# Performance work log

Hardware: AMD Instinct MI355X
Metric: run time of the kernel (lower is better)

The kernel has to match this reference:

```python
import jax, jax.numpy as jnp
import numpy as np
import math

HEAD_NUM = 16


def setup_inputs() -> dict:
    key = jax.random.key(0)
    ks = jax.random.split(key, 6)
    B, S, E = 2, 2048, 1024
    sc = 1.0 / math.sqrt(E)
    return {
        "x": jax.random.normal(ks[0], (B, S, E), dtype=jnp.float32),
        "mask": jnp.ones((B, S), dtype=jnp.int32),
        "Wq": jax.random.normal(ks[1], (E, E), dtype=jnp.float32) * sc,
        "bq": jnp.zeros((E,), dtype=jnp.float32),
        "Wk": jax.random.normal(ks[2], (E, E), dtype=jnp.float32) * sc,
        "bk": jnp.zeros((E,), dtype=jnp.float32),
        "Wv": jax.random.normal(ks[3], (E, E), dtype=jnp.float32) * sc,
        "bv": jnp.zeros((E,), dtype=jnp.float32),
        "Wo": jax.random.normal(ks[4], (E, E), dtype=jnp.float32) * sc,
        "bo": jnp.zeros((E,), dtype=jnp.float32),
    }


def reference(x, mask, Wq, bq, Wk, bk, Wv, bv, Wo, bo):
    B, S, E = x.shape
    H = HEAD_NUM
    D = E // H
    # Projections (nn.Linear: x @ W^T + b; W here stored so that x @ W is equivalent)
    q = (x @ Wq + bq).reshape(B, S, H, D).transpose(0, 2, 1, 3)  # [B,H,S,D]
    k = (x @ Wk + bk).reshape(B, S, H, D).transpose(0, 2, 1, 3)
    v = (x @ Wv + bv).reshape(B, S, H, D).transpose(0, 2, 1, 3)
    score = jnp.einsum("bhqd,bhkd->bhqk", q, k) / jnp.sqrt(jnp.asarray(D, x.dtype))
    # Faithful to source: masked positions (mask==0) are filled with +inf
    m = mask[:, None, None, :]  # [B,1,1,S]
    score = jnp.where(m == 0, jnp.inf, score)
    attn = jax.nn.softmax(score, axis=-1)
    # dropout is identity in eval mode
    out = jnp.einsum("bhqk,bhkd->bhqd", attn, v)
    out = out.transpose(0, 2, 1, 3).reshape(B, S, E)
    return out @ Wo + bo
```

## Files before the change

### kernel.cpp

```cpp
#include <hip/hip_runtime.h>
#include <hip/hip_bf16.h>
#include <math.h>


#define S_LEN 2048
#define EMB   1024
#define HN    16
#define HD    64
#define BATCH 2
#define MROWS (BATCH * S_LEN)
#define NEL   ((size_t)MROWS * EMB)

typedef _Float16 f16x8 __attribute__((ext_vector_type(8)));
typedef _Float16 f16x4 __attribute__((ext_vector_type(4)));
typedef _Float16 f16x2 __attribute__((ext_vector_type(2)));
typedef float    f32x4  __attribute__((ext_vector_type(4)));
typedef float    f32x16 __attribute__((ext_vector_type(16)));
typedef unsigned u32x4  __attribute__((ext_vector_type(4)));

#define GLOAD_LDS16(g, l) \
  __builtin_amdgcn_global_load_lds((const __attribute__((address_space(1))) void*)(g), \
                                   (__attribute__((address_space(3))) void*)(l), 16, 0, 0)

__device__ __forceinline__ float exp2fast(float x) {
#if __has_builtin(__builtin_amdgcn_exp2f)
  return __builtin_amdgcn_exp2f(x);
#else
  return __expf(x * 0.69314718056f);
#endif
}

__device__ __forceinline__ unsigned pk_f16(float a, float b) {
#if __has_builtin(__builtin_amdgcn_cvt_pkrtz)
  auto h = __builtin_amdgcn_cvt_pkrtz(a, b);
  return __builtin_bit_cast(unsigned, h);
#else
  unsigned lo = (unsigned)__builtin_bit_cast(unsigned short, (_Float16)a);
  unsigned hi = (unsigned)__builtin_bit_cast(unsigned short, (_Float16)b);
  return lo | (hi << 16);
#endif
}

__device__ __forceinline__ float dot2acc(unsigned p, float acc) {
#if __has_builtin(__builtin_amdgcn_fdot2)
  f16x2 ones = {(_Float16)1.0f, (_Float16)1.0f};
  return __builtin_amdgcn_fdot2(__builtin_bit_cast(f16x2, p), ones, acc, false);
#else
  f16x2 v = __builtin_bit_cast(f16x2, p);
  return acc + (float)v[0] + (float)v[1];
#endif
}

__device__ __forceinline__ f32x16 mfma32(f16x8 a, f16x8 b, f32x16 c) {
  return __builtin_amdgcn_mfma_f32_32x32x16_f16(a, b, c, 0, 0, 0);
}

__global__ __launch_bounds__(256)
void prep_f16(const float* __restrict__ x,
              const float* __restrict__ Wq, const float* __restrict__ Wk,
              const float* __restrict__ Wv, const float* __restrict__ Wo,
              _Float16* __restrict__ xf, _Float16* __restrict__ Wt,
              _Float16* __restrict__ Wot) {
  __shared__ float tile[64][65];
  const int bid = blockIdx.x;
  const int tt  = threadIdx.x;
  if (bid < 2048) {
    const int i = bid * 256 + tt;
    const float4* s = (const float4*)x + (size_t)i * 2;
    float4 a = s[0], b = s[1];
    f16x8 o = {(_Float16)a.x, (_Float16)a.y, (_Float16)a.z, (_Float16)a.w,
               (_Float16)b.x, (_Float16)b.y, (_Float16)b.z, (_Float16)b.w};
    *((f16x8*)xf + i) = o;
    return;
  }
  const int j   = bid - 2048;
  const int job = j >> 8;
  const int tl  = j & 255;
  const int bn  = (tl & 15) * 64, bk = (tl >> 4) * 64;
  const float* W = (job == 0) ? Wq : (job == 1) ? Wk : (job == 2) ? Wv : Wo;
  _Float16* dst = (job == 3) ? Wot : Wt + (size_t)job * EMB * EMB;
  const int c = tt & 63, r4 = tt >> 6;
#pragma unroll
  for (int jj = 0; jj < 16; ++jj) {
    int r = r4 * 16 + jj;
    tile[r][c] = W[(size_t)(bk + r) * EMB + bn + c];
  }
  __syncthreads();
#pragma unroll
  for (int jj = 0; jj < 16; ++jj) {
    int rr = r4 * 16 + jj;
    dst[(size_t)(bn + rr) * EMB + bk + c] = (_Float16)tile[c][rr];
  }
}

template<bool SW>
__device__ __forceinline__ void gemm_kloop(
    const _Float16* __restrict__ gA, const _Float16* __restrict__ gB,
    _Float16* As, _Float16* Bs, int tid, int wr, int wc, int ql, int hi,
    f32x16 (&acc)[2][2]) {
#define GSTAGE(buf, k0) do { \
    _Pragma("unroll") \
    for (int j = 0; j < 2; ++j) { \
      const int c = tid + j * 256; \
      const int row = c >> 2; \
      const int sl = ((c & 3) ^ (row & 3) ^ ((row >> 2) & 3)) * 8; \
      GLOAD_LDS16(gA + (size_t)row * EMB + (k0) + sl, As + (buf) * 4096 + c * 8); \
      GLOAD_LDS16(gB + (size_t)row * EMB + (k0) + sl, Bs + (buf) * 4096 + c * 8); \
    } \
  } while (0)
#define GCOMP(bufc) do { \
    const _Float16* Ab = As + (bufc) * 4096; \
    const _Float16* Bb = Bs + (bufc) * 4096; \
    _Pragma("unroll") \
    for (int ks = 0; ks < 2; ++ks) { \
      const int sl = ((((ks << 1) | hi) ^ (ql & 3) ^ ((ql >> 2) & 3)) << 3); \
      f16x8 a0 = *(const f16x8*)&Ab[(wr * 64 + ql) * 32 + sl]; \
      f16x8 a1 = *(const f16x8*)&Ab[(wr * 64 + 32 + ql) * 32 + sl]; \
      f16x8 b0 = *(const f16x8*)&Bb[(wc * 64 + ql) * 32 + sl]; \
      f16x8 b1 = *(const f16x8*)&Bb[(wc * 64 + 32 + ql) * 32 + sl]; \
      if (SW) { \
        acc[0][0] = mfma32(b0, a0, acc[0][0]); \
        acc[0][1] = mfma32(b1, a0, acc[0][1]); \
        acc[1][0] = mfma32(b0, a1, acc[1][0]); \
        acc[1][1] = mfma32(b1, a1, acc[1][1]); \
      } else { \
        acc[0][0] = mfma32(a0, b0, acc[0][0]); \
        acc[0][1] = mfma32(a0, b1, acc[0][1]); \
        acc[1][0] = mfma32(a1, b0, acc[1][0]); \
        acc[1][1] = mfma32(a1, b1, acc[1][1]); \
      } \
    } \
  } while (0)

  GSTAGE(0, 0);
  GSTAGE(1, 32);
  int cur = 0, stg = 2;
#pragma unroll 1
  for (int t = 0; t < 31; ++t) {
    asm volatile("s_waitcnt vmcnt(4) lgkmcnt(0)" ::: "memory");
    __builtin_amdgcn_sched_barrier(0);
    __builtin_amdgcn_s_barrier();
    __builtin_amdgcn_sched_barrier(0);
    if (t < 30) GSTAGE(stg, (t + 2) * 32);
    GCOMP(cur);
    cur = (cur == 2) ? 0 : cur + 1;
    stg = (stg == 2) ? 0 : stg + 1;
  }
  asm volatile("s_waitcnt vmcnt(0) lgkmcnt(0)" ::: "memory");
  __builtin_amdgcn_sched_barrier(0);
  __builtin_amdgcn_s_barrier();
  __builtin_amdgcn_sched_barrier(0);
  GCOMP(cur);
#undef GCOMP
#undef GSTAGE
}

template<int MODE>
__global__ __launch_bounds__(256, 3)
void gemm_f16(const _Float16* __restrict__ A, const _Float16* __restrict__ Bt,
              int Ncols,
              _Float16* __restrict__ qf, _Float16* __restrict__ kf,
              _Float16* __restrict__ vf, float* __restrict__ outF,
              const float* __restrict__ b0, const float* __restrict__ b1,
              const float* __restrict__ b2) {
  __shared__ _Float16 As[3 * 128 * 32];
  __shared__ _Float16 Bs[3 * 128 * 32];
  const int tid  = threadIdx.x;
  const int lane = tid & 63, w = tid >> 6;
  const int ql = lane & 31, hi = lane >> 5;
  const int wr = w >> 1, wc = w & 1;

  const int nbx  = Ncols >> 7;
  const int ncpx = nbx >> 3;
  const int xcd  = blockIdx.x & 7;
  const int idx  = blockIdx.x >> 3;
  const int col0 = (xcd * ncpx + idx % ncpx) << 7;
  const int row0 = (idx / ncpx) << 7;

  f32x16 acc[2][2];
#pragma unroll
  for (int mi = 0; mi < 2; ++mi)
#pragma unroll
    for (int ni = 0; ni < 2; ++ni) acc[mi][ni] = (f32x16){};

  const _Float16* gA = A  + (size_t)row0 * EMB;
  const _Float16* gB = Bt + (size_t)col0 * EMB;

  const bool is_v = (MODE == 0) && (col0 >= 2048);
  if (is_v) gemm_kloop<true >(gA, gB, As, Bs, tid, wr, wc, ql, hi, acc);
  else      gemm_kloop<false>(gA, gB, As, Bs, tid, wr, wc, ql, hi, acc);

  if (MODE == 1) {
#pragma unroll
    for (int mi = 0; mi < 2; ++mi)
#pragma unroll
      for (int ni = 0; ni < 2; ++ni) {
        const int n = col0 + wc * 64 + ni * 32 + ql;
        const float bias = b0[n];
#pragma unroll
        for (int r = 0; r < 16; ++r) {
          const int m = row0 + wr * 64 + mi * 32 + (r & 3) + 8 * (r >> 2) + 4 * hi;
          outF[(size_t)m * EMB + n] = acc[mi][ni][r] + bias;
        }
      }
  } else if (!is_v) {
#pragma unroll
    for (int mi = 0; mi < 2; ++mi)
#pragma unroll
      for (int ni = 0; ni < 2; ++ni) {
        const int n = col0 + wc * 64 + ni * 32 + ql;
        const int mat = n >> 10, e = n & 1023;
        const float bias = (mat == 0 ? b0 : b1)[e];
        const int h = e >> 6, d = e & 63;
#pragma unroll
        for (int r = 0; r < 16; ++r) {
          const int m = row0 + wr * 64 + mi * 32 + (r & 3) + 8 * (r >> 2) + 4 * hi;
          const int bb = m >> 11, ss = m & 2047;
          const int bh = bb * HN + h;
          float val = acc[mi][ni][r] + bias;
          if (mat == 0) {
            qf[((size_t)bh * S_LEN + ss) * HD + d] = (_Float16)(val * 0.18033688f);
          } else {
            kf[((size_t)bh * S_LEN + ss) * HD + d] = (_Float16)val;
          }
        }
      }
  } else {
#pragma unroll
    for (int mi = 0; mi < 2; ++mi) {
      const int m = row0 + wr * 64 + mi * 32 + ql;
      const int bb = m >> 11, ss = m & 2047;
      const int ssp = (ss & ~12) | ((ss & 4) << 1) | ((ss & 8) >> 1);
#pragma unroll
      for (int ni = 0; ni < 2; ++ni) {
#pragma unroll
        for (int r = 0; r < 16; ++r) {
          const int n = col0 + wc * 64 + ni * 32 + (r & 3) + 8 * (r >> 2) + 4 * hi;
          const int e = n - 2048;
          const int h = e >> 6, d = e & 63;
          const int bh = bb * HN + h;
          float val = acc[mi][ni][r] + b2[e];
          vf[((size_t)bh * HD + d) * S_LEN + ssp] = (_Float16)val;
        }
      }
    }
  }
}

__global__ __launch_bounds__(512)
void attn_f16v5(const _Float16* __restrict__ Qf, const _Float16* __restrict__ Kf,
                const _Float16* __restrict__ VfT, _Float16* __restrict__ Of) {
  __shared__ _Float16 SH[2][4][4096];

  const int tid  = threadIdx.x;
  const int lane = tid & 63, w = tid >> 6;
  const int ws4  = w & 3, ks = w >> 2;
  const int ql = lane & 31;
  const int hi = lane >> 5;

  const int logical = ((blockIdx.x & 7) << 6) | (blockIdx.x >> 3);
  const int bh = logical >> 4;
  const int qc = logical & 15;
  const int q0w = (qc << 7) + (ws4 << 5);
  const int kbase = ks << 10;

  const size_t qbase = ((size_t)bh * S_LEN + q0w + ql) * HD + hi * 8;
  f16x8 qa[4];
#pragma unroll
  for (int ds = 0; ds < 4; ++ds) qa[ds] = *(const f16x8*)&Qf[qbase + ds * 16];

  f32x16 o0 = {}, o1 = {};
  float lsum = 0.f;

  const int cA = (ws4 << 6) + lane, cB = cA + 256;
  const int rA = cA >> 3, sA = ((cA & 7) ^ (rA & 7)) * 8;
  const int rB = cB >> 3, sB = ((cB & 7) ^ (rB & 7)) * 8;
  const _Float16* KB = Kf  + (size_t)bh * S_LEN * HD;
  const _Float16* VB = VfT + (size_t)bh * HD * S_LEN;

#pragma unroll 1
  for (int t = 0; t < 8; ++t) {
    const int k0 = kbase + t * 128;
    __syncthreads();
    GLOAD_LDS16(KB + (size_t)(k0 + rA) * HD + sA,       &SH[ks][0][cA * 8]);
    GLOAD_LDS16(KB + (size_t)(k0 + rB) * HD + sB,       &SH[ks][0][cB * 8]);
    GLOAD_LDS16(KB + (size_t)(k0 + 64 + rA) * HD + sA,  &SH[ks][1][cA * 8]);
    GLOAD_LDS16(KB + (size_t)(k0 + 64 + rB) * HD + sB,  &SH[ks][1][cB * 8]);
    GLOAD_LDS16(VB + (size_t)rA * S_LEN + k0 + sA,      &SH[ks][2][cA * 8]);
    GLOAD_LDS16(VB + (size_t)rB * S_LEN + k0 + sB,      &SH[ks][2][cB * 8]);
    GLOAD_LDS16(VB + (size_t)rA * S_LEN + k0 + 64 + sA, &SH[ks][3][cA * 8]);
    GLOAD_LDS16(VB + (size_t)rB * S_LEN + k0 + 64 + sB, &SH[ks][3][cB * 8]);
    __syncthreads();

#pragma unroll
    for (int kh = 0; kh < 2; ++kh) {
      const _Float16* Kt = &SH[ks][kh][0];
      const _Float16* Vt = &SH[ks][2 + kh][0];
      f32x16 sf0 = {}, sf1 = {};
#pragma unroll
      for (int ds = 0; ds < 4; ++ds) {
        const int sl = ((ds * 2 + hi) ^ (ql & 7)) * 8;
        f16x8 ka0 = *(const f16x8*)&Kt[ql * 64 + sl];
        f16x8 ka1 = *(const f16x8*)&Kt[(32 + ql) * 64 + sl];
        sf0 = mfma32(ka0, qa[ds], sf0);
        sf1 = mfma32(ka1, qa[ds], sf1);
      }

      unsigned wv[16];
#pragma unroll
      for (int i = 0; i < 8; ++i) {
        float p0 = exp2fast(sf0[2 * i]), p1 = exp2fast(sf0[2 * i + 1]);
        float p2 = exp2fast(sf1[2 * i]), p3 = exp2fast(sf1[2 * i + 1]);
        wv[i]     = pk_f16(p0, p1);
        wv[8 + i] = pk_f16(p2, p3);
        lsum = dot2acc(wv[i], lsum);
        lsum = dot2acc(wv[8 + i], lsum);
      }

#pragma unroll
      for (int kq = 0; kq < 4; ++kq) {
        u32x4 pw = {wv[4 * kq], wv[4 * kq + 1], wv[4 * kq + 2], wv[4 * kq + 3]};
        f16x8 pb = __builtin_bit_cast(f16x8, pw);
        const int sl = ((kq * 2 + hi) ^ (ql & 7)) * 8;
        f16x8 va0 = *(const f16x8*)&Vt[ql * 64 + sl];
        f16x8 va1 = *(const f16x8*)&Vt[(32 + ql) * 64 + sl];
        o0 = mfma32(va0, pb, o0);
        o1 = mfma32(va1, pb, o1);
      }
    }
  }

  __syncthreads();
  float* CMB = reinterpret_cast<float*>(&SH[0][0][0]);
  float* slot = CMB + ((size_t)((ws4 << 6) + lane)) * 36;
  if (ks == 1) {
#pragma unroll
    for (int t = 0; t < 4; ++t) {
      *(f32x4*)&slot[4 * t] =
          (f32x4){o0[4 * t], o0[4 * t + 1], o0[4 * t + 2], o0[4 * t + 3]};
      *(f32x4*)&slot[16 + 4 * t] =
          (f32x4){o1[4 * t], o1[4 * t + 1], o1[4 * t + 2], o1[4 * t + 3]};
    }
    slot[32] = lsum;
  }
  __syncthreads();
  if (ks == 0) {
#pragma unroll
    for (int t = 0; t < 4; ++t) {
      f32x4 a0 = *(const f32x4*)&slot[4 * t];
      f32x4 a1 = *(const f32x4*)&slot[16 + 4 * t];
#pragma unroll
      for (int j = 0; j < 4; ++j) { o0[4 * t + j] += a0[j]; o1[4 * t + j] += a1[j]; }
    }
    lsum += slot[32];
    float lt  = lsum + __shfl_xor(lsum, 32);
    float inv = 1.0f / lt;
    const int b = bh >> 4, h = bh & 15;
    _Float16* ob = Of + ((size_t)(b * S_LEN + q0w + ql)) * EMB + (h << 6);
#pragma unroll
    for (int t = 0; t < 4; ++t) {
      f16x4 v0, v1;
#pragma unroll
      for (int j = 0; j < 4; ++j) {
        v0[j] = (_Float16)(o0[4 * t + j] * inv);
        v1[j] = (_Float16)(o1[4 * t + j] * inv);
      }
      *(f16x4*)&ob[8 * t + 4 * hi]      = v0;
      *(f16x4*)&ob[32 + 8 * t + 4 * hi] = v1;
    }
  }
}


extern "C" void kernel_launch(void* const* d_in, const int* in_sizes, int n_in,
                              void* d_out, int out_size, void* d_ws, size_t ws_size,
                              hipStream_t stream) {
  const float* x  = (const float*)d_in[0];
  const float* Wq = (const float*)d_in[2];
  const float* bq = (const float*)d_in[3];
  const float* Wk = (const float*)d_in[4];
  const float* bk = (const float*)d_in[5];
  const float* Wv = (const float*)d_in[6];
  const float* bv = (const float*)d_in[7];
  const float* Wo = (const float*)d_in[8];
  const float* bo = (const float*)d_in[9];
  float* out = (float*)d_out;

  _Float16* Qf  = (_Float16*)d_ws;
  _Float16* Kf  = Qf + NEL;
  _Float16* VfT = Kf + NEL;
  _Float16* xf  = VfT + NEL;
  _Float16* Of  = xf;
  _Float16* Wt  = xf + NEL;
  _Float16* Wot = Wt + 3 * (size_t)EMB * EMB;

  prep_f16<<<dim3(3072), 256, 0, stream>>>(x, Wq, Wk, Wv, Wo, xf, Wt, Wot);

  gemm_f16<0><<<dim3((MROWS / 128) * (3072 / 128)), 256, 0, stream>>>(
      xf, Wt, 3072, Qf, Kf, VfT, nullptr, bq, bk, bv);

  attn_f16v5<<<dim3(BATCH * HN * (S_LEN / 128)), 512, 0, stream>>>(
      Qf, Kf, VfT, Of);

  gemm_f16<1><<<dim3((MROWS / 128) * (EMB / 128)), 256, 0, stream>>>(
      Of, Wot, 1024, nullptr, nullptr, nullptr, out, bo, nullptr, nullptr);
}
```

Before: 115.3 us.

## Load K tiles directly into registers instead of staging through LDS

The attention kernel now reads K fragments straight from global memory into registers, and prefetches the second half-tile of K during the first half's compute. Only V is staged through shared memory, which halves LDS usage and the number of async LDS loads per iteration. The softmax row-sum is also split into two independent accumulators to shorten the dependency chain. In exchange, every wave reads K from global/L2 separately with no cross-wave reuse, and register pressure rises.

```diff
diff --git a/kernel.cpp b/kernel.cpp
--- a/kernel.cpp
+++ b/kernel.cpp
@@ -248,9 +248,9 @@
 }
 
 __global__ __launch_bounds__(512)
-void attn_f16v5(const _Float16* __restrict__ Qf, const _Float16* __restrict__ Kf,
+void attn_f16v8(const _Float16* __restrict__ Qf, const _Float16* __restrict__ Kf,
                 const _Float16* __restrict__ VfT, _Float16* __restrict__ Of) {
-  __shared__ _Float16 SH[2][4][4096];
+  __shared__ _Float16 SH[2][2][4608];
 
   const int tid  = threadIdx.x;
   const int lane = tid & 63, w = tid >> 6;
@@ -270,40 +270,54 @@
   for (int ds = 0; ds < 4; ++ds) qa[ds] = *(const f16x8*)&Qf[qbase + ds * 16];
 
   f32x16 o0 = {}, o1 = {};
-  float lsum = 0.f;
+  float lsum0 = 0.f, lsum1 = 0.f;
 
   const int cA = (ws4 << 6) + lane, cB = cA + 256;
   const int rA = cA >> 3, sA = ((cA & 7) ^ (rA & 7)) * 8;
   const int rB = cB >> 3, sB = ((cB & 7) ^ (rB & 7)) * 8;
   const _Float16* KB = Kf  + (size_t)bh * S_LEN * HD;
   const _Float16* VB = VfT + (size_t)bh * HD * S_LEN;
+  const int dofs = hi * 8;
 
 #pragma unroll 1
   for (int t = 0; t < 8; ++t) {
     const int k0 = kbase + t * 128;
+
+    const _Float16* K0 = KB + (size_t)(k0 + ql) * HD + dofs;
+    const _Float16* K1 = KB + (size_t)(k0 + 32 + ql) * HD + dofs;
+    f16x8 kA[4], kB4[4];
+#pragma unroll
+    for (int ds = 0; ds < 4; ++ds) {
+      kA[ds]  = *(const f16x8*)&K0[ds * 16];
+      kB4[ds] = *(const f16x8*)&K1[ds * 16];
+    }
+
     __syncthreads();
-    GLOAD_LDS16(KB + (size_t)(k0 + rA) * HD + sA,       &SH[ks][0][cA * 8]);
-    GLOAD_LDS16(KB + (size_t)(k0 + rB) * HD + sB,       &SH[ks][0][cB * 8]);
-    GLOAD_LDS16(KB + (size_t)(k0 + 64 + rA) * HD + sA,  &SH[ks][1][cA * 8]);
-    GLOAD_LDS16(KB + (size_t)(k0 + 64 + rB) * HD + sB,  &SH[ks][1][cB * 8]);
-    GLOAD_LDS16(VB + (size_t)rA * S_LEN + k0 + sA,      &SH[ks][2][cA * 8]);
-    GLOAD_LDS16(VB + (size_t)rB * S_LEN + k0 + sB,      &SH[ks][2][cB * 8]);
-    GLOAD_LDS16(VB + (size_t)rA * S_LEN + k0 + 64 + sA, &SH[ks][3][cA * 8]);
-    GLOAD_LDS16(VB + (size_t)rB * S_LEN + k0 + 64 + sB, &SH[ks][3][cB * 8]);
+    GLOAD_LDS16(VB + (size_t)rA * S_LEN + k0 + sA,      &SH[ks][0][cA * 8]);
+    GLOAD_LDS16(VB + (size_t)rB * S_LEN + k0 + sB,      &SH[ks][0][cB * 8]);
+    GLOAD_LDS16(VB + (size_t)rA * S_LEN + k0 + 64 + sA, &SH[ks][1][cA * 8]);
+    GLOAD_LDS16(VB + (size_t)rB * S_LEN + k0 + 64 + sB, &SH[ks][1][cB * 8]);
     __syncthreads();
 
 #pragma unroll
     for (int kh = 0; kh < 2; ++kh) {
-      const _Float16* Kt = &SH[ks][kh][0];
-      const _Float16* Vt = &SH[ks][2 + kh][0];
+      const _Float16* Vt = &SH[ks][kh][0];
+
       f32x16 sf0 = {}, sf1 = {};
 #pragma unroll
       for (int ds = 0; ds < 4; ++ds) {
-        const int sl = ((ds * 2 + hi) ^ (ql & 7)) * 8;
-        f16x8 ka0 = *(const f16x8*)&Kt[ql * 64 + sl];
-        f16x8 ka1 = *(const f16x8*)&Kt[(32 + ql) * 64 + sl];
-        sf0 = mfma32(ka0, qa[ds], sf0);
-        sf1 = mfma32(ka1, qa[ds], sf1);
+        sf0 = mfma32(kA[ds],  qa[ds], sf0);
+        sf1 = mfma32(kB4[ds], qa[ds], sf1);
+      }
+
+      if (kh == 0) {
+        const _Float16* K2 = KB + (size_t)(k0 + 64 + ql) * HD + dofs;
+        const _Float16* K3 = KB + (size_t)(k0 + 96 + ql) * HD + dofs;
+#pragma unroll
+        for (int ds = 0; ds < 4; ++ds) {
+          kA[ds]  = *(const f16x8*)&K2[ds * 16];
+          kB4[ds] = *(const f16x8*)&K3[ds * 16];
+        }
       }
 
       unsigned wv[16];
@@ -313,8 +327,8 @@
         float p2 = exp2fast(sf1[2 * i]), p3 = exp2fast(sf1[2 * i + 1]);
         wv[i]     = pk_f16(p0, p1);
         wv[8 + i] = pk_f16(p2, p3);
-        lsum = dot2acc(wv[i], lsum);
-        lsum = dot2acc(wv[8 + i], lsum);
+        lsum0 = dot2acc(wv[i], lsum0);
+        lsum1 = dot2acc(wv[8 + i], lsum1);
       }
 
 #pragma unroll
@@ -329,6 +343,7 @@
       }
     }
   }
+  float lsum = lsum0 + lsum1;
 
   __syncthreads();
   float* CMB = reinterpret_cast<float*>(&SH[0][0][0]);
@@ -399,7 +414,7 @@
   gemm_f16<0><<<dim3((MROWS / 128) * (3072 / 128)), 256, 0, stream>>>(
       xf, Wt, 3072, Qf, Kf, VfT, nullptr, bq, bk, bv);
 
-  attn_f16v5<<<dim3(BATCH * HN * (S_LEN / 128)), 512, 0, stream>>>(
+  attn_f16v8<<<dim3(BATCH * HN * (S_LEN / 128)), 512, 0, stream>>>(
       Qf, Kf, VfT, Of);
 
   gemm_f16<1><<<dim3((MROWS / 128) * (EMB / 128)), 256, 0, stream>>>(
```

Result: slower. 155.7 us (+35.0%).
